# Optimization experiments

Measured on AMD Instinct MI355X. Metric: run time of the kernel, lower is better.

## Reference

```python
import jax, jax.numpy as jnp
import numpy as np

B, IN_NUM, IN_DIM = 64, 4096, 8
NUM_CAPS, DIM_CAPS, ROUTINGS = 32, 16, 3
EPS = 1e-7  # keras.backend.epsilon()


def squash(v, axis=-1):
    # squash(s) = ||s||^2/(1+||s||^2) * s/||s||
    s2 = jnp.sum(v * v, axis=axis, keepdims=True)
    return (s2 / (1.0 + s2)) * v / jnp.sqrt(s2 + EPS)


def setup_inputs() -> dict:
    key = jax.random.key(0)
    k1, k2 = jax.random.split(key)
    inputs = jax.random.normal(k1, (B, IN_NUM, IN_DIM), dtype=jnp.float32)
    # kernel: [num_capsule, input_num_capsule, dim_capsule, input_dim_capsule]
    W = jax.random.normal(k2, (NUM_CAPS, IN_NUM, DIM_CAPS, IN_DIM), dtype=jnp.float32) * 0.05
    return {"inputs": inputs, "W": W}


def reference(inputs, W):
    # prediction vectors u_hat[b,c,n,j] = sum_i W[c,n,j,i] * x[b,n,i]
    hat = jnp.einsum('bni,cnji->bcnj', inputs, W)  # [B, C, N, D]
    b = jnp.zeros(hat.shape[:3], hat.dtype)        # routing logits [B, C, N]
    out = None
    for i in range(ROUTINGS):
        c = jax.nn.softmax(b, axis=1)              # couple over output capsules
        out = squash(jnp.einsum('bcn,bcnj->bcj', c, hat))  # [B, C, D]
        if i < ROUTINGS - 1:
            b = b + jnp.einsum('bcj,bcnj->bcn', out, hat)  # agreement update
    return out
```

## Files before the change

kernel.cpp:

```cpp
#include <hip/hip_runtime.h>
#include <math.h>


typedef __fp16 h2 __attribute__((ext_vector_type(2)));
typedef __fp16 half4 __attribute__((ext_vector_type(4)));
typedef float f32x16 __attribute__((ext_vector_type(16)));

union U2 { h2 h; unsigned u; };

__device__ __forceinline__ float fdot2(h2 a, h2 b, float c) {
    return __builtin_amdgcn_fdot2(a, b, c, false);
}
__device__ __forceinline__ h2 uash2(unsigned u) { U2 t; t.u = u; return t.h; }

template <int PASS0, int NPB>
__global__ __launch_bounds__(512, 4) void fused_pass(
    const float* __restrict__ W,
    const float* __restrict__ x,
    ushort* __restrict__ Wh,
    const ushort* __restrict__ OcumG,
    unsigned* __restrict__ partial)
{
    constexpr int NB = 4096 / NPB;
    const int bid = blockIdx.x;
    const int bt = bid / NB, nblk = bid % NB;
    const int n0 = nblk * NPB;
    const int t = threadIdx.x, l = t & 63, w = t >> 6;
    const int bl = l & 31, hi = l >> 5;
    const int b = bt * 32 + bl;

    __shared__ __align__(16) float pd[2][32][12];
    __shared__ unsigned sep[8192];

    const int cj0 = w * 64 + bl, cj1 = cj0 + 32;
    const float* xb = x + (size_t)b * 32768 + (size_t)n0 * 8 + hi * 4;
    const float* wb0 = W + (size_t)(cj0 >> 4) * 524288 + (size_t)n0 * 128 + (cj0 & 15) * 8 + hi * 4;
    const float* wb1 = W + (size_t)(cj1 >> 4) * 524288 + (size_t)n0 * 128 + (cj1 & 15) * 8 + hi * 4;
    ushort* whp0 = Wh + ((size_t)n0 * 512 + cj0) * 8 + hi * 4;
    ushort* whp1 = Wh + ((size_t)n0 * 512 + cj1) * 8 + hi * 4;

    h2 oc[2][8];
    if (!PASS0) {
        const unsigned* og = reinterpret_cast<const unsigned*>(OcumG);
        #pragma unroll
        for (int mt = 0; mt < 2; ++mt) {
            const int cA = 4 * w + 2 * mt;
            const unsigned idx = (unsigned)b * 256 + cA * 8 + hi * 2;
            oc[mt][0] = uash2(og[idx]);      oc[mt][1] = uash2(og[idx + 1]);
            oc[mt][2] = uash2(og[idx + 4]);  oc[mt][3] = uash2(og[idx + 5]);
            oc[mt][4] = uash2(og[idx + 8]);  oc[mt][5] = uash2(og[idx + 9]);
            oc[mt][6] = uash2(og[idx + 12]); oc[mt][7] = uash2(og[idx + 13]);
        }
    }

    f32x16 zero = {};
    f32x16 acc0 = {}, acc1 = {};

    if (PASS0) {
        float4 wv0 = *reinterpret_cast<const float4*>(wb0);
        float4 wv1 = *reinterpret_cast<const float4*>(wb1);
        float4 xv  = *reinterpret_cast<const float4*>(xb);
        #pragma unroll 1
        for (int s = 0; s < NPB; ++s) {
            float4 wv0n, wv1n, xvn;
            if (s < NPB - 1) {
                wv0n = *reinterpret_cast<const float4*>(wb0 + (s + 1) * 128);
                wv1n = *reinterpret_cast<const float4*>(wb1 + (s + 1) * 128);
                xvn  = *reinterpret_cast<const float4*>(xb + (s + 1) * 8);
            }
            half4 a0, a1, bf;
            a0[0] = (__fp16)wv0.x; a0[1] = (__fp16)wv0.y; a0[2] = (__fp16)wv0.z; a0[3] = (__fp16)wv0.w;
            a1[0] = (__fp16)wv1.x; a1[1] = (__fp16)wv1.y; a1[2] = (__fp16)wv1.z; a1[3] = (__fp16)wv1.w;
            bf[0] = (__fp16)xv.x;  bf[1] = (__fp16)xv.y;  bf[2] = (__fp16)xv.z;  bf[3] = (__fp16)xv.w;
            if (bt == 0) {
                *reinterpret_cast<half4*>(whp0 + (size_t)s * 4096) = a0;
                *reinterpret_cast<half4*>(whp1 + (size_t)s * 4096) = a1;
            }
            acc0 = __builtin_amdgcn_mfma_f32_32x32x8f16(a0, bf, acc0, 0, 0, 0);
            acc1 = __builtin_amdgcn_mfma_f32_32x32x8f16(a1, bf, acc1, 0, 0, 0);
            wv0 = wv0n; wv1 = wv1n; xv = xvn;
        }
        #pragma unroll
        for (int r = 0; r < 16; ++r) { acc0[r] *= 0.03125f; acc1[r] *= 0.03125f; }
    } else {
        half4 a0 = *reinterpret_cast<const half4*>(whp0);
        half4 a1 = *reinterpret_cast<const half4*>(whp1);
        float4 xv = *reinterpret_cast<const float4*>(xb);
        #pragma unroll 1
        for (int s = 0; s < NPB; ++s) {
            half4 a0n, a1n; float4 xvn;
            if (s < NPB - 1) {
                a0n = *reinterpret_cast<const half4*>(whp0 + (size_t)(s + 1) * 4096);
                a1n = *reinterpret_cast<const half4*>(whp1 + (size_t)(s + 1) * 4096);
                xvn = *reinterpret_cast<const float4*>(xb + (s + 1) * 8);
            }
            half4 bf;
            bf[0] = (__fp16)xv.x; bf[1] = (__fp16)xv.y; bf[2] = (__fp16)xv.z; bf[3] = (__fp16)xv.w;
            f32x16 d0 = __builtin_amdgcn_mfma_f32_32x32x8f16(a0, bf, zero, 0, 0, 0);
            f32x16 d1 = __builtin_amdgcn_mfma_f32_32x32x8f16(a1, bf, zero, 0, 0, 0);
            h2 h0[8], h1[8];
            #pragma unroll
            for (int q = 0; q < 8; ++q) {
                h0[q] = __builtin_amdgcn_cvt_pkrtz(d0[2 * q], d0[2 * q + 1]);
                h1[q] = __builtin_amdgcn_cvt_pkrtz(d1[2 * q], d1[2 * q + 1]);
            }
            float pA0 = fdot2(h0[3], oc[0][3], fdot2(h0[2], oc[0][2], fdot2(h0[1], oc[0][1], fdot2(h0[0], oc[0][0], 0.f))));
            float pB0 = fdot2(h0[7], oc[0][7], fdot2(h0[6], oc[0][6], fdot2(h0[5], oc[0][5], fdot2(h0[4], oc[0][4], 0.f))));
            float pA1 = fdot2(h1[3], oc[1][3], fdot2(h1[2], oc[1][2], fdot2(h1[1], oc[1][1], fdot2(h1[0], oc[1][0], 0.f))));
            float pB1 = fdot2(h1[7], oc[1][7], fdot2(h1[6], oc[1][6], fdot2(h1[5], oc[1][5], fdot2(h1[4], oc[1][4], 0.f))));
            pA0 += __shfl_xor(pA0, 32, 64);
            pB0 += __shfl_xor(pB0, 32, 64);
            pA1 += __shfl_xor(pA1, 32, 64);
            pB1 += __shfl_xor(pB1, 32, 64);
            float eA0 = __expf(pA0), eB0 = __expf(pB0), eA1 = __expf(pA1), eB1 = __expf(pB1);
            const int buf = s & 1;
            if (l < 32) pd[buf][bl][w] = eA0 + eB0 + eA1 + eB1;
            __syncthreads();
            const float4 q0 = *reinterpret_cast<const float4*>(&pd[buf][bl][0]);
            const float4 q1 = *reinterpret_cast<const float4*>(&pd[buf][bl][4]);
            const float rd = __builtin_amdgcn_rcpf(q0.x + q0.y + q0.z + q0.w +
                                                   q1.x + q1.y + q1.z + q1.w);
            const float cA0 = eA0 * rd, cB0 = eB0 * rd, cA1 = eA1 * rd, cB1 = eB1 * rd;
            #pragma unroll
            for (int r = 0; r < 8; ++r)  { acc0[r] += d0[r] * cA0; acc1[r] += d1[r] * cA1; }
            #pragma unroll
            for (int r = 8; r < 16; ++r) { acc0[r] += d0[r] * cB0; acc1[r] += d1[r] * cB1; }
            a0 = a0n; a1 = a1n; xv = xvn;
        }
    }

    __syncthreads();
    #pragma unroll
    for (int mt = 0; mt < 2; ++mt) {
        #pragma unroll
        for (int q = 0; q < 8; ++q) {
            const float e0 = mt ? acc1[2 * q] : acc0[2 * q];
            const float e1 = mt ? acc1[2 * q + 1] : acc0[2 * q + 1];
            U2 u; u.h = __builtin_amdgcn_cvt_pkrtz(e0, e1);
            const int cjp = w * 32 + mt * 16 + 4 * (q >> 1) + (q & 1) + 2 * hi;
            sep[bl * 256 + (cjp ^ bl)] = u.u;
        }
    }
    __syncthreads();
    const unsigned gbase = (unsigned)bid * 8192;
    #pragma unroll
    for (int u2 = 0; u2 < 16; ++u2) {
        const int idx = t + u2 * 512;
        const int ubl = idx >> 8, ucjp = idx & 255;
        partial[gbase + idx] = sep[ubl * 256 + (ucjp ^ ubl)];
    }
}


template <int NB>
__global__ __launch_bounds__(256) void reduce_squash(const unsigned* __restrict__ partial32,
                                                     ushort* __restrict__ OcumG,
                                                     float* __restrict__ out,
                                                     int passIdx) {
    const int tid = blockIdx.x * 256 + threadIdx.x;
    const int b = tid >> 8, cjp = tid & 255;
    const int bt = b >> 5, bl = b & 31;
    const unsigned base = (unsigned)bt * (unsigned)NB * 8192u + (unsigned)bl * 256u + (unsigned)cjp;
    float sx = 0.f, sy = 0.f;
    #pragma unroll 8
    for (int nb = 0; nb < NB; ++nb) {
        U2 v; v.u = partial32[base + nb * 8192];
        sx += (float)v.h.x;
        sy += (float)v.h.y;
    }
    float s2 = sx * sx + sy * sy;
    s2 += __shfl_xor(s2, 1, 64);
    s2 += __shfl_xor(s2, 2, 64);
    s2 += __shfl_xor(s2, 4, 64);
    float scale = (s2 / (1.f + s2)) / sqrtf(s2 + 1e-7f);
    float o0 = scale * sx, o1 = scale * sy;

    unsigned* ocp = reinterpret_cast<unsigned*>(OcumG) + b * 256 + cjp;
    float a0 = o0, a1 = o1;
    if (passIdx) {
        U2 old; old.u = *ocp;
        a0 += (float)old.h.x;
        a1 += (float)old.h.y;
    }
    U2 nw; nw.h = __builtin_amdgcn_cvt_pkrtz(a0, a1);
    *ocp = nw.u;

    if (passIdx == 2) {
        out[b * 512 + cjp * 2] = o0;
        out[b * 512 + cjp * 2 + 1] = o1;
    }
}


extern "C" void kernel_launch(void* const* d_in, const int* in_sizes, int n_in,
                              void* d_out, int out_size, void* d_ws, size_t ws_size,
                              hipStream_t stream) {
    const float* x = (const float*)d_in[0];
    const float* W = (const float*)d_in[1];
    float* out = (float*)d_out;

    char* ws = (char*)d_ws;
    ushort* Wh = (ushort*)ws;

    const size_t MiB = 1024 * 1024;
    if (ws_size >= 48 * MiB + 65536) {
        unsigned* partialU = (unsigned*)(ws + 32 * MiB);
        ushort* OcumG = (ushort*)(ws + 48 * MiB);
        for (int pass = 0; pass < 3; ++pass) {
            if (pass == 0)
                fused_pass<1, 16><<<512, 512, 0, stream>>>(W, x, Wh, OcumG, partialU);
            else
                fused_pass<0, 16><<<512, 512, 0, stream>>>(W, x, Wh, OcumG, partialU);
            reduce_squash<256><<<64, 256, 0, stream>>>(partialU, OcumG, out, pass);
        }
    } else {
        unsigned* partialU = (unsigned*)(ws + 32 * MiB);
        ushort* OcumG = (ushort*)(ws + 40 * MiB);
        for (int pass = 0; pass < 3; ++pass) {
            if (pass == 0)
                fused_pass<1, 32><<<256, 512, 0, stream>>>(W, x, Wh, OcumG, partialU);
            else
                fused_pass<0, 32><<<256, 512, 0, stream>>>(W, x, Wh, OcumG, partialU);
            reduce_squash<128><<<64, 256, 0, stream>>>(partialU, OcumG, out, pass);
        }
    }
}
```

Measured before the change: 206.3 us.

## Split pass0 into W-once kernel, cache fp16 x, widen reduce parallelism

Pass 0 gets its own kernel in which each block covers all 64 batches for half the output capsules. Each W element is read and converted to fp16 exactly once, where before every batch tile re-read it, and the kernel also writes an fp16 copy of x in an n-major layout. Passes 1 and 2 then read the fp16 x, halving x traffic and dropping the per-step conversion. The reduce kernel splits each output across 4 threads with shuffle reductions, raising its grid from 64 to 256 blocks. The cost is an extra fp16 x buffer in the workspace and a scattered partial-write pattern in pass 0.

```diff
diff --git a/kernel.cpp b/kernel.cpp
--- a/kernel.cpp
+++ b/kernel.cpp
@@ -13,11 +13,86 @@
 }
 __device__ __forceinline__ h2 uash2(unsigned u) { U2 t; t.u = u; return t.h; }
 
-template <int PASS0, int NPB>
-__global__ __launch_bounds__(512, 4) void fused_pass(
+
+template <int NPB>
+__global__ __launch_bounds__(512, 4) void pass0_kernel(
     const float* __restrict__ W,
     const float* __restrict__ x,
     ushort* __restrict__ Wh,
+    ushort* __restrict__ xh,
+    unsigned* __restrict__ partial)
+{
+    constexpr int NB = 4096 / NPB;
+    const int bid = blockIdx.x;
+    const int half = bid / NB, nblk = bid % NB;
+    const int n0 = nblk * NPB;
+    const int t = threadIdx.x, l = t & 63, w = t >> 6;
+    const int bl = l & 31, hi = l >> 5;
+    const int cj = half * 256 + w * 32 + bl;
+
+    __shared__ unsigned sep[8192];
+
+    const float* wb  = W + (size_t)(cj >> 4) * 524288 + (size_t)n0 * 128 + (cj & 15) * 8 + hi * 4;
+    const float* xb0 = x + (size_t)bl * 32768 + (size_t)n0 * 8 + hi * 4;
+    const float* xb1 = x + (size_t)(bl + 32) * 32768 + (size_t)n0 * 8 + hi * 4;
+    ushort* whp = Wh + ((size_t)n0 * 512 + cj) * 8 + hi * 4;
+    ushort* xhp = xh + ((size_t)n0 * 64 + bl) * 8 + hi * 4;
+
+    f32x16 acc0 = {}, acc1 = {};
+    float4 wv  = *reinterpret_cast<const float4*>(wb);
+    float4 xv0 = *reinterpret_cast<const float4*>(xb0);
+    float4 xv1 = *reinterpret_cast<const float4*>(xb1);
+    #pragma unroll 1
+    for (int s = 0; s < NPB; ++s) {
+        float4 wvn, x0n, x1n;
+        if (s < NPB - 1) {
+            wvn = *reinterpret_cast<const float4*>(wb + (s + 1) * 128);
+            x0n = *reinterpret_cast<const float4*>(xb0 + (s + 1) * 8);
+            x1n = *reinterpret_cast<const float4*>(xb1 + (s + 1) * 8);
+        }
+        half4 a, b0, b1;
+        a[0] = (__fp16)wv.x;  a[1] = (__fp16)wv.y;  a[2] = (__fp16)wv.z;  a[3] = (__fp16)wv.w;
+        b0[0] = (__fp16)xv0.x; b0[1] = (__fp16)xv0.y; b0[2] = (__fp16)xv0.z; b0[3] = (__fp16)xv0.w;
+        b1[0] = (__fp16)xv1.x; b1[1] = (__fp16)xv1.y; b1[2] = (__fp16)xv1.z; b1[3] = (__fp16)xv1.w;
+        *reinterpret_cast<half4*>(whp + (size_t)s * 4096) = a;
+        if (w == 0) {
+            *reinterpret_cast<half4*>(xhp + (size_t)s * 512) = b0;
+            *reinterpret_cast<half4*>(xhp + (size_t)s * 512 + 256) = b1;
+        }
+        acc0 = __builtin_amdgcn_mfma_f32_32x32x8f16(a, b0, acc0, 0, 0, 0);
+        acc1 = __builtin_amdgcn_mfma_f32_32x32x8f16(a, b1, acc1, 0, 0, 0);
+        wv = wvn; xv0 = x0n; xv1 = x1n;
+    }
+    #pragma unroll
+    for (int r = 0; r < 16; ++r) { acc0[r] *= 0.03125f; acc1[r] *= 0.03125f; }
+
+    #pragma unroll
+    for (int hb = 0; hb < 2; ++hb) {
+        #pragma unroll
+        for (int q = 0; q < 8; ++q) {
+            const float e0 = hb ? acc1[2 * q] : acc0[2 * q];
+            const float e1 = hb ? acc1[2 * q + 1] : acc0[2 * q + 1];
+            U2 u; u.h = __builtin_amdgcn_cvt_pkrtz(e0, e1);
+            const int cjp = w * 16 + 4 * (q >> 1) + (q & 1) + 2 * hi;
+            const int bb = bl + 32 * hb;
+            sep[bb * 128 + (cjp ^ bb)] = u.u;
+        }
+    }
+    __syncthreads();
+    #pragma unroll
+    for (int u2 = 0; u2 < 16; ++u2) {
+        const int idx = t + u2 * 512;
+        const int ub = idx >> 7, ucjp = idx & 127;
+        partial[(size_t)((ub >> 5) * NB + nblk) * 8192 + (ub & 31) * 256 + half * 128 + ucjp]
+            = sep[ub * 128 + (ucjp ^ ub)];
+    }
+}
+
+
+template <int NPB>
+__global__ __launch_bounds__(512, 4) void pass12_kernel(
+    const ushort* __restrict__ Wh,
+    const ushort* __restrict__ xh,
     const ushort* __restrict__ OcumG,
     unsigned* __restrict__ partial)
 {
@@ -33,14 +108,12 @@
     __shared__ unsigned sep[8192];
 
     const int cj0 = w * 64 + bl, cj1 = cj0 + 32;
-    const float* xb = x + (size_t)b * 32768 + (size_t)n0 * 8 + hi * 4;
-    const float* wb0 = W + (size_t)(cj0 >> 4) * 524288 + (size_t)n0 * 128 + (cj0 & 15) * 8 + hi * 4;
-    const float* wb1 = W + (size_t)(cj1 >> 4) * 524288 + (size_t)n0 * 128 + (cj1 & 15) * 8 + hi * 4;
-    ushort* whp0 = Wh + ((size_t)n0 * 512 + cj0) * 8 + hi * 4;
-    ushort* whp1 = Wh + ((size_t)n0 * 512 + cj1) * 8 + hi * 4;
+    const ushort* xb = xh + ((size_t)n0 * 64 + b) * 8 + hi * 4;
+    const ushort* whp0 = Wh + ((size_t)n0 * 512 + cj0) * 8 + hi * 4;
+    const ushort* whp1 = Wh + ((size_t)n0 * 512 + cj1) * 8 + hi * 4;
 
     h2 oc[2][8];
-    if (!PASS0) {
+    {
         const unsigned* og = reinterpret_cast<const unsigned*>(OcumG);
         #pragma unroll
         for (int mt = 0; mt < 2; ++mt) {
@@ -56,77 +129,47 @@
     f32x16 zero = {};
     f32x16 acc0 = {}, acc1 = {};
 
-    if (PASS0) {
-        float4 wv0 = *reinterpret_cast<const float4*>(wb0);
-        float4 wv1 = *reinterpret_cast<const float4*>(wb1);
-        float4 xv  = *reinterpret_cast<const float4*>(xb);
-        #pragma unroll 1
-        for (int s = 0; s < NPB; ++s) {
-            float4 wv0n, wv1n, xvn;
-            if (s < NPB - 1) {
-                wv0n = *reinterpret_cast<const float4*>(wb0 + (s + 1) * 128);
-                wv1n = *reinterpret_cast<const float4*>(wb1 + (s + 1) * 128);
-                xvn  = *reinterpret_cast<const float4*>(xb + (s + 1) * 8);
-            }
-            half4 a0, a1, bf;
-            a0[0] = (__fp16)wv0.x; a0[1] = (__fp16)wv0.y; a0[2] = (__fp16)wv0.z; a0[3] = (__fp16)wv0.w;
-            a1[0] = (__fp16)wv1.x; a1[1] = (__fp16)wv1.y; a1[2] = (__fp16)wv1.z; a1[3] = (__fp16)wv1.w;
-            bf[0] = (__fp16)xv.x;  bf[1] = (__fp16)xv.y;  bf[2] = (__fp16)xv.z;  bf[3] = (__fp16)xv.w;
-            if (bt == 0) {
-                *reinterpret_cast<half4*>(whp0 + (size_t)s * 4096) = a0;
-                *reinterpret_cast<half4*>(whp1 + (size_t)s * 4096) = a1;
-            }
-            acc0 = __builtin_amdgcn_mfma_f32_32x32x8f16(a0, bf, acc0, 0, 0, 0);
-            acc1 = __builtin_amdgcn_mfma_f32_32x32x8f16(a1, bf, acc1, 0, 0, 0);
-            wv0 = wv0n; wv1 = wv1n; xv = xvn;
-        }
-        #pragma unroll
-        for (int r = 0; r < 16; ++r) { acc0[r] *= 0.03125f; acc1[r] *= 0.03125f; }
-    } else {
-        half4 a0 = *reinterpret_cast<const half4*>(whp0);
-        half4 a1 = *reinterpret_cast<const half4*>(whp1);
-        float4 xv = *reinterpret_cast<const float4*>(xb);
-        #pragma unroll 1
-        for (int s = 0; s < NPB; ++s) {
-            half4 a0n, a1n; float4 xvn;
-            if (s < NPB - 1) {
-                a0n = *reinterpret_cast<const half4*>(whp0 + (size_t)(s + 1) * 4096);
-                a1n = *reinterpret_cast<const half4*>(whp1 + (size_t)(s + 1) * 4096);
-                xvn = *reinterpret_cast<const float4*>(xb + (s + 1) * 8);
-            }
-            half4 bf;
-            bf[0] = (__fp16)xv.x; bf[1] = (__fp16)xv.y; bf[2] = (__fp16)xv.z; bf[3] = (__fp16)xv.w;
-            f32x16 d0 = __builtin_amdgcn_mfma_f32_32x32x8f16(a0, bf, zero, 0, 0, 0);
-            f32x16 d1 = __builtin_amdgcn_mfma_f32_32x32x8f16(a1, bf, zero, 0, 0, 0);
-            h2 h0[8], h1[8];
-            #pragma unroll
-            for (int q = 0; q < 8; ++q) {
-                h0[q] = __builtin_amdgcn_cvt_pkrtz(d0[2 * q], d0[2 * q + 1]);
-                h1[q] = __builtin_amdgcn_cvt_pkrtz(d1[2 * q], d1[2 * q + 1]);
-            }
-            float pA0 = fdot2(h0[3], oc[0][3], fdot2(h0[2], oc[0][2], fdot2(h0[1], oc[0][1], fdot2(h0[0], oc[0][0], 0.f))));
-            float pB0 = fdot2(h0[7], oc[0][7], fdot2(h0[6], oc[0][6], fdot2(h0[5], oc[0][5], fdot2(h0[4], oc[0][4], 0.f))));
-            float pA1 = fdot2(h1[3], oc[1][3], fdot2(h1[2], oc[1][2], fdot2(h1[1], oc[1][1], fdot2(h1[0], oc[1][0], 0.f))));
-            float pB1 = fdot2(h1[7], oc[1][7], fdot2(h1[6], oc[1][6], fdot2(h1[5], oc[1][5], fdot2(h1[4], oc[1][4], 0.f))));
-            pA0 += __shfl_xor(pA0, 32, 64);
-            pB0 += __shfl_xor(pB0, 32, 64);
-            pA1 += __shfl_xor(pA1, 32, 64);
-            pB1 += __shfl_xor(pB1, 32, 64);
-            float eA0 = __expf(pA0), eB0 = __expf(pB0), eA1 = __expf(pA1), eB1 = __expf(pB1);
-            const int buf = s & 1;
-            if (l < 32) pd[buf][bl][w] = eA0 + eB0 + eA1 + eB1;
-            __syncthreads();
-            const float4 q0 = *reinterpret_cast<const float4*>(&pd[buf][bl][0]);
-            const float4 q1 = *reinterpret_cast<const float4*>(&pd[buf][bl][4]);
-            const float rd = __builtin_amdgcn_rcpf(q0.x + q0.y + q0.z + q0.w +
-                                                   q1.x + q1.y + q1.z + q1.w);
-            const float cA0 = eA0 * rd, cB0 = eB0 * rd, cA1 = eA1 * rd, cB1 = eB1 * rd;
-            #pragma unroll
-            for (int r = 0; r < 8; ++r)  { acc0[r] += d0[r] * cA0; acc1[r] += d1[r] * cA1; }
-            #pragma unroll
-            for (int r = 8; r < 16; ++r) { acc0[r] += d0[r] * cB0; acc1[r] += d1[r] * cB1; }
-            a0 = a0n; a1 = a1n; xv = xvn;
-        }
+    half4 a0 = *reinterpret_cast<const half4*>(whp0);
+    half4 a1 = *reinterpret_cast<const half4*>(whp1);
+    half4 bf = *reinterpret_cast<const half4*>(xb);
+    #pragma unroll 1
+    for (int s = 0; s < NPB; ++s) {
+        half4 a0n, a1n, bfn;
+        if (s < NPB - 1) {
+            a0n = *reinterpret_cast<const half4*>(whp0 + (size_t)(s + 1) * 4096);
+            a1n = *reinterpret_cast<const half4*>(whp1 + (size_t)(s + 1) * 4096);
+            bfn = *reinterpret_cast<const half4*>(xb + (size_t)(s + 1) * 512);
+        }
+        f32x16 d0 = __builtin_amdgcn_mfma_f32_32x32x8f16(a0, bf, zero, 0, 0, 0);
+        f32x16 d1 = __builtin_amdgcn_mfma_f32_32x32x8f16(a1, bf, zero, 0, 0, 0);
+        h2 h0[8], h1[8];
+        #pragma unroll
+        for (int q = 0; q < 8; ++q) {
+            h0[q] = __builtin_amdgcn_cvt_pkrtz(d0[2 * q], d0[2 * q + 1]);
+            h1[q] = __builtin_amdgcn_cvt_pkrtz(d1[2 * q], d1[2 * q + 1]);
+        }
+        float pA0 = fdot2(h0[3], oc[0][3], fdot2(h0[2], oc[0][2], fdot2(h0[1], oc[0][1], fdot2(h0[0], oc[0][0], 0.f))));
+        float pB0 = fdot2(h0[7], oc[0][7], fdot2(h0[6], oc[0][6], fdot2(h0[5], oc[0][5], fdot2(h0[4], oc[0][4], 0.f))));
+        float pA1 = fdot2(h1[3], oc[1][3], fdot2(h1[2], oc[1][2], fdot2(h1[1], oc[1][1], fdot2(h1[0], oc[1][0], 0.f))));
+        float pB1 = fdot2(h1[7], oc[1][7], fdot2(h1[6], oc[1][6], fdot2(h1[5], oc[1][5], fdot2(h1[4], oc[1][4], 0.f))));
+        pA0 += __shfl_xor(pA0, 32, 64);
+        pB0 += __shfl_xor(pB0, 32, 64);
+        pA1 += __shfl_xor(pA1, 32, 64);
+        pB1 += __shfl_xor(pB1, 32, 64);
+        float eA0 = __expf(pA0), eB0 = __expf(pB0), eA1 = __expf(pA1), eB1 = __expf(pB1);
+        const int buf = s & 1;
+        if (l < 32) pd[buf][bl][w] = eA0 + eB0 + eA1 + eB1;
+        __syncthreads();
+        const float4 q0 = *reinterpret_cast<const float4*>(&pd[buf][bl][0]);
+        const float4 q1 = *reinterpret_cast<const float4*>(&pd[buf][bl][4]);
+        const float rd = __builtin_amdgcn_rcpf(q0.x + q0.y + q0.z + q0.w +
+                                               q1.x + q1.y + q1.z + q1.w);
+        const float cA0 = eA0 * rd, cB0 = eB0 * rd, cA1 = eA1 * rd, cB1 = eB1 * rd;
+        #pragma unroll
+        for (int r = 0; r < 8; ++r)  { acc0[r] += d0[r] * cA0; acc1[r] += d1[r] * cA1; }
+        #pragma unroll
+        for (int r = 8; r < 16; ++r) { acc0[r] += d0[r] * cB0; acc1[r] += d1[r] * cB1; }
+        a0 = a0n; a1 = a1n; bf = bfn;
     }
 
     __syncthreads();
@@ -157,37 +200,41 @@
                                                      ushort* __restrict__ OcumG,
                                                      float* __restrict__ out,
                                                      int passIdx) {
-    const int tid = blockIdx.x * 256 + threadIdx.x;
-    const int b = tid >> 8, cjp = tid & 255;
+    const int gtid = blockIdx.x * 256 + threadIdx.x;
+    const int oid = gtid >> 2, sub = gtid & 3;
+    const int b = oid >> 8, cjp = oid & 255;
     const int bt = b >> 5, bl = b & 31;
     const unsigned base = (unsigned)bt * (unsigned)NB * 8192u + (unsigned)bl * 256u + (unsigned)cjp;
     float sx = 0.f, sy = 0.f;
     #pragma unroll 8
-    for (int nb = 0; nb < NB; ++nb) {
-        U2 v; v.u = partial32[base + nb * 8192];
+    for (int i = 0; i < NB / 4; ++i) {
+        U2 v; v.u = partial32[base + (unsigned)(sub + 4 * i) * 8192u];
         sx += (float)v.h.x;
         sy += (float)v.h.y;
     }
+    sx += __shfl_xor(sx, 1, 64); sy += __shfl_xor(sy, 1, 64);
+    sx += __shfl_xor(sx, 2, 64); sy += __shfl_xor(sy, 2, 64);
     float s2 = sx * sx + sy * sy;
-    s2 += __shfl_xor(s2, 1, 64);
-    s2 += __shfl_xor(s2, 2, 64);
     s2 += __shfl_xor(s2, 4, 64);
+    s2 += __shfl_xor(s2, 8, 64);
+    s2 += __shfl_xor(s2, 16, 64);
     float scale = (s2 / (1.f + s2)) / sqrtf(s2 + 1e-7f);
     float o0 = scale * sx, o1 = scale * sy;
 
-    unsigned* ocp = reinterpret_cast<unsigned*>(OcumG) + b * 256 + cjp;
-    float a0 = o0, a1 = o1;
-    if (passIdx) {
-        U2 old; old.u = *ocp;
-        a0 += (float)old.h.x;
-        a1 += (float)old.h.y;
-    }
-    U2 nw; nw.h = __builtin_amdgcn_cvt_pkrtz(a0, a1);
-    *ocp = nw.u;
-
-    if (passIdx == 2) {
-        out[b * 512 + cjp * 2] = o0;
-        out[b * 512 + cjp * 2 + 1] = o1;
+    if (sub == 0) {
+        unsigned* ocp = reinterpret_cast<unsigned*>(OcumG) + b * 256 + cjp;
+        float a0 = o0, a1 = o1;
+        if (passIdx) {
+            U2 old; old.u = *ocp;
+            a0 += (float)old.h.x;
+            a1 += (float)old.h.y;
+        }
+        U2 nw; nw.h = __builtin_amdgcn_cvt_pkrtz(a0, a1);
+        *ocp = nw.u;
+        if (passIdx == 2) {
+            out[b * 512 + cjp * 2] = o0;
+            out[b * 512 + cjp * 2 + 1] = o1;
+        }
     }
 }
 
@@ -201,27 +248,27 @@
 
     char* ws = (char*)d_ws;
     ushort* Wh = (ushort*)ws;
-
     const size_t MiB = 1024 * 1024;
-    if (ws_size >= 48 * MiB + 65536) {
+
+    if (ws_size >= 52 * MiB + 65536) {
         unsigned* partialU = (unsigned*)(ws + 32 * MiB);
-        ushort* OcumG = (ushort*)(ws + 48 * MiB);
-        for (int pass = 0; pass < 3; ++pass) {
-            if (pass == 0)
-                fused_pass<1, 16><<<512, 512, 0, stream>>>(W, x, Wh, OcumG, partialU);
-            else
-                fused_pass<0, 16><<<512, 512, 0, stream>>>(W, x, Wh, OcumG, partialU);
-            reduce_squash<256><<<64, 256, 0, stream>>>(partialU, OcumG, out, pass);
-        }
+        ushort* xh = (ushort*)(ws + 48 * MiB);
+        ushort* OcumG = (ushort*)(ws + 52 * MiB);
+        pass0_kernel<16><<<512, 512, 0, stream>>>(W, x, Wh, xh, partialU);
+        reduce_squash<256><<<256, 256, 0, stream>>>(partialU, OcumG, out, 0);
+        pass12_kernel<16><<<512, 512, 0, stream>>>(Wh, xh, OcumG, partialU);
+        reduce_squash<256><<<256, 256, 0, stream>>>(partialU, OcumG, out, 1);
+        pass12_kernel<16><<<512, 512, 0, stream>>>(Wh, xh, OcumG, partialU);
+        reduce_squash<256><<<256, 256, 0, stream>>>(partialU, OcumG, out, 2);
     } else {
         unsigned* partialU = (unsigned*)(ws + 32 * MiB);
-        ushort* OcumG = (ushort*)(ws + 40 * MiB);
-        for (int pass = 0; pass < 3; ++pass) {
-            if (pass == 0)
-                fused_pass<1, 32><<<256, 512, 0, stream>>>(W, x, Wh, OcumG, partialU);
-            else
-                fused_pass<0, 32><<<256, 512, 0, stream>>>(W, x, Wh, OcumG, partialU);
-            reduce_squash<128><<<64, 256, 0, stream>>>(partialU, OcumG, out, pass);
-        }
-    }
-}
+        ushort* xh = (ushort*)(ws + 40 * MiB);
+        ushort* OcumG = (ushort*)(ws + 44 * MiB);
+        pass0_kernel<32><<<256, 512, 0, stream>>>(W, x, Wh, xh, partialU);
+        reduce_squash<128><<<256, 256, 0, stream>>>(partialU, OcumG, out, 0);
+        pass12_kernel<32><<<256, 512, 0, stream>>>(Wh, xh, OcumG, partialU);
+        reduce_squash<128><<<256, 256, 0, stream>>>(partialU, OcumG, out, 1);
+        pass12_kernel<32><<<256, 512, 0, stream>>>(Wh, xh, OcumG, partialU);
+        reduce_squash<128><<<256, 256, 0, stream>>>(partialU, OcumG, out, 2);
+    }
+}
```

Measured after the change: 180.9 us. -12.3%, faster.
